# Performance work log

Measured on AMD Instinct MI355X. Metric: run time of the kernel, lower is better.

Reference implementation:

```python
import jax, jax.numpy as jnp
import numpy as np

N_NODES = 50000
N_EDGES = 800000
IN_CH = 128
OUT_CH = 64
HEADS = 4
NEG_SLOPE = 0.2


def setup_inputs() -> dict:
    key = jax.random.key(0)
    k1, k2, k3, k4, k5, k6 = jax.random.split(key, 6)
    x = jax.random.normal(k1, (N_NODES, IN_CH), dtype=jnp.float32)
    edge_index = jax.random.randint(k2, (2, N_EDGES), 0, N_NODES, dtype=jnp.int64)
    # GATConv params (glorot-ish scale)
    W = jax.random.normal(k3, (HEADS * OUT_CH, IN_CH), dtype=jnp.float32) * (1.0 / np.sqrt(IN_CH))
    att_src = jax.random.normal(k4, (HEADS, OUT_CH), dtype=jnp.float32) * 0.1
    att_dst = jax.random.normal(k5, (HEADS, OUT_CH), dtype=jnp.float32) * 0.1
    bias = jax.random.normal(k6, (HEADS * OUT_CH,), dtype=jnp.float32) * 0.01
    return {"x": x, "edge_index": edge_index, "W": W, "att_src": att_src, "att_dst": att_dst, "bias": bias}


def reference(x, edge_index, W, att_src, att_dst, bias):
    N = x.shape[0]
    H, C = att_src.shape
    # add self loops (PyG GATConv default add_self_loops=True)
    loops = jnp.arange(N, dtype=edge_index.dtype)
    src = jnp.concatenate([edge_index[0], loops])  # [E+N]
    dst = jnp.concatenate([edge_index[1], loops])
    # linear projection -> [N, H, C]
    xl = (x @ W.T).reshape(N, H, C)
    # per-node attention logits [N, H]
    a_src = jnp.einsum('nhc,hc->nh', xl, att_src)
    a_dst = jnp.einsum('nhc,hc->nh', xl, att_dst)
    # edge-wise score, leaky relu
    alpha = jax.nn.leaky_relu(a_src[src] + a_dst[dst], NEG_SLOPE)  # [E+N, H]
    # segment softmax over destination nodes (every node has a self loop -> no empty segments)
    amax = jax.ops.segment_max(alpha, dst, num_segments=N)
    e = jnp.exp(alpha - amax[dst])
    denom = jax.ops.segment_sum(e, dst, num_segments=N)
    coef = e / denom[dst]  # [E+N, H]
    # weighted scatter-aggregate of source features
    out = jax.ops.segment_sum(coef[:, :, None] * xl[src], dst, num_segments=N)  # [N, H, C]
    out = out.reshape(N, H * C) + bias
    # last_layer=False -> ELU activation
    return jax.nn.elu(out)
```

## Files before the change

### kernel.cpp

```cpp
#include <hip/hip_runtime.h>
#include <hip/hip_bf16.h>
#include <math.h>

#define IN_C 128
#define HC   256
#define CH   64
#define NEG  0.2f

typedef __attribute__((ext_vector_type(8))) short short8;
typedef __attribute__((ext_vector_type(4))) float f32x4;
typedef __attribute__((ext_vector_type(2))) float f32x2;

#define TSTRIDE 264

__device__ __forceinline__ float lrelu(float v) { return v > 0.f ? v : NEG * v; }

__device__ __forceinline__ unsigned short f2bf(float f) {
    __hip_bfloat16 h = __float2bfloat16(f);
    return *reinterpret_cast<unsigned short*>(&h);
}
__device__ __forceinline__ unsigned pack2(float lo, float hi) {
    return (unsigned)f2bf(lo) | ((unsigned)f2bf(hi) << 16);
}

__device__ __forceinline__ void fma8pk(f32x2* acc, float wf, const uint4 u) {
    const f32x2 w2 = {wf, wf};
    f32x2 b;
    b.x = __uint_as_float(u.x << 16); b.y = __uint_as_float(u.x & 0xFFFF0000u);
    acc[0] = __builtin_elementwise_fma(w2, b, acc[0]);
    b.x = __uint_as_float(u.y << 16); b.y = __uint_as_float(u.y & 0xFFFF0000u);
    acc[1] = __builtin_elementwise_fma(w2, b, acc[1]);
    b.x = __uint_as_float(u.z << 16); b.y = __uint_as_float(u.z & 0xFFFF0000u);
    acc[2] = __builtin_elementwise_fma(w2, b, acc[2]);
    b.x = __uint_as_float(u.w << 16); b.y = __uint_as_float(u.w & 0xFFFF0000u);
    acc[3] = __builtin_elementwise_fma(w2, b, acc[3]);
}

__global__ void k_wconv(const float* __restrict__ W, short* __restrict__ Wb, int n)
{
    int i = blockIdx.x * 256 + threadIdx.x;
    if (i * 4 >= n) return;
    const float4 v = *(const float4*)&W[i * 4];
    uint2 pk;
    pk.x = pack2(v.x, v.y);
    pk.y = pack2(v.z, v.w);
    *(uint2*)&Wb[i * 4] = pk;
}

__global__ void __launch_bounds__(256) k_gemm_deg(
    const float* __restrict__ x, const short* __restrict__ Wb,
    const float* __restrict__ att_src, const float* __restrict__ att_dst,
    const int* __restrict__ ei, int* __restrict__ deg, int* __restrict__ perm,
    __hip_bfloat16* __restrict__ xlb, float* __restrict__ asrc,
    float* __restrict__ adst, int N, int E, int DB)
{
    __shared__ short Wlds[256 * 128];

    const int t = threadIdx.x;

    if ((int)blockIdx.x < DB) {
        const int stride = DB * 256;
        for (int e = blockIdx.x * 256 + t; e < E; e += stride) {
            const int d = ei[E + e];
            perm[e] = atomicAdd(&deg[d], 1);
        }
        return;
    }

    const int bx   = blockIdx.x - DB;
    const int wv   = t >> 6;
    const int lane = t & 63;
    const int m    = lane & 15;
    const int quad = lane >> 4;
    const int r0   = bx * 64 + wv * 16;

#pragma unroll
    for (int i = 0; i < 16; ++i) {
        const int g   = t + 256 * i;
        const int row = g >> 4;
        const int c   = g & 15;
        const uint4 v = *(const uint4*)&Wb[g * 8];
        *(uint4*)&Wlds[row * 128 + ((c ^ (row & 15)) * 8)] = v;
    }
    __syncthreads();

    f32x4 acc[16];
#pragma unroll
    for (int tc = 0; tc < 16; ++tc) acc[tc] = (f32x4){0.f, 0.f, 0.f, 0.f};

    const int arow = min(r0 + m, N - 1);
    const float* xrow = &x[(size_t)arow * IN_C];

#pragma unroll
    for (int kc = 0; kc < IN_C; kc += 32) {
        union { short8 v; unsigned u[4]; } a;
        const float4 xa = *(const float4*)&xrow[kc + quad * 8];
        const float4 xb = *(const float4*)&xrow[kc + quad * 8 + 4];
        a.u[0] = pack2(xa.x, xa.y); a.u[1] = pack2(xa.z, xa.w);
        a.u[2] = pack2(xb.x, xb.y); a.u[3] = pack2(xb.z, xb.w);
        const int kchunk = (kc >> 3) + quad;
        const int slotoff = ((kchunk ^ m) * 8);
#pragma unroll
        for (int tc = 0; tc < 16; ++tc) {
            const short8 b = *(const short8*)&Wlds[(tc * 16 + m) * 128 + slotoff];
            acc[tc] = __builtin_amdgcn_mfma_f32_16x16x32_bf16(a.v, b, acc[tc], 0, 0, 0);
        }
    }

    float as_l[16], ad_l[16];
#pragma unroll
    for (int tc = 0; tc < 16; ++tc) {
        as_l[tc] = att_src[tc * 16 + m];
        ad_l[tc] = att_dst[tc * 16 + m];
    }
#pragma unroll
    for (int i = 0; i < 4; ++i) {
        const int grow = r0 + quad * 4 + i;
        const bool ok = grow < N;
        float ps[4] = {0.f, 0.f, 0.f, 0.f};
        float pd[4] = {0.f, 0.f, 0.f, 0.f};
#pragma unroll
        for (int tc = 0; tc < 16; ++tc) {
            const float v = acc[tc][i];
            ps[tc >> 2] = fmaf(v, as_l[tc], ps[tc >> 2]);
            pd[tc >> 2] = fmaf(v, ad_l[tc], pd[tc >> 2]);
        }
#pragma unroll
        for (int msk = 1; msk < 16; msk <<= 1) {
#pragma unroll
            for (int hd = 0; hd < 4; ++hd) {
                ps[hd] += __shfl_xor(ps[hd], msk);
                pd[hd] += __shfl_xor(pd[hd], msk);
            }
        }
        if (m == 0 && ok) {
#pragma unroll
            for (int hd = 0; hd < 4; ++hd) {
                asrc[grow * 4 + hd] = ps[hd];
                adst[grow * 4 + hd] = pd[hd];
            }
        }
    }

    __syncthreads();
#pragma unroll
    for (int i = 0; i < 4; ++i) {
        const int lrow = wv * 16 + quad * 4 + i;
#pragma unroll
        for (int tc = 0; tc < 16; ++tc)
            Wlds[lrow * TSTRIDE + tc * 16 + m] = (short)f2bf(acc[tc][i]);
    }
    __syncthreads();
    const int r0blk = bx * 64;
#pragma unroll
    for (int k2 = 0; k2 < 8; ++k2) {
        const int c   = t + 256 * k2;
        const int row = c >> 5;
        const int off = c & 31;
        if (r0blk + row < N) {
            const uint4 v = *(const uint4*)&Wlds[row * TSTRIDE + off * 8];
            *(uint4*)&xlb[(size_t)(r0blk + row) * HC + off * 8] = v;
        }
    }
}

__global__ void k_scan1(const int* __restrict__ deg, int* __restrict__ offs,
                        int* __restrict__ partials, int N)
{
    __shared__ int sh[1024];
    int t = threadIdx.x, b = blockIdx.x;
    int idx = b * 1024 + t;
    int v = (idx < N) ? deg[idx] : 0;
    sh[t] = v; __syncthreads();
    for (int off = 1; off < 1024; off <<= 1) {
        int u = (t >= off) ? sh[t - off] : 0;
        __syncthreads();
        sh[t] += u;
        __syncthreads();
    }
    if (idx < N) offs[idx] = sh[t] - v;
    if (t == 1023) partials[b] = sh[t];
}

__global__ void k_scan2(int* __restrict__ partials, int nparts)
{
    __shared__ int sh[1024];
    int t = threadIdx.x;
    int v = (t < nparts) ? partials[t] : 0;
    sh[t] = v; __syncthreads();
    for (int off = 1; off < 1024; off <<= 1) {
        int u = (t >= off) ? sh[t - off] : 0;
        __syncthreads();
        sh[t] += u;
        __syncthreads();
    }
    if (t < nparts) partials[t] = sh[t] - v;
}

__global__ void k_scan3(int* __restrict__ offs, const int* __restrict__ partials,
                        int N, int E)
{
    int t = threadIdx.x, b = blockIdx.x;
    int idx = b * 1024 + t;
    if (idx < N) offs[idx] += partials[b];
    if (idx == 0) offs[N] = E;
}

__global__ void k_place(const int* __restrict__ ei, const int* __restrict__ perm,
                        const int* __restrict__ offs, int* __restrict__ csr_src, int E)
{
    int e = blockIdx.x * 256 + threadIdx.x;
    if (e >= E) return;
    int s = ei[e];
    int d = ei[E + e];
    csr_src[offs[d] + perm[e]] = s;
}

__global__ void __launch_bounds__(256, 8) k_agg(
    const __hip_bfloat16* __restrict__ xlb, const float* __restrict__ asrc,
    const float* __restrict__ adst, const int* __restrict__ offs,
    const int* __restrict__ csr_src, const float* __restrict__ bias,
    float* __restrict__ out, int N)
{
    const int t    = threadIdx.x;
    const int wv   = t >> 6;
    const int lane = t & 63;
    const int half = lane >> 5;
    const int li   = lane & 31;
    const int h    = li >> 3;
    const int n    = blockIdx.x * 4 + wv;
    if (n >= N) return;

    const float adn = adst[n * 4 + h];
    const int   p0 = offs[n];
    const int   pe = offs[n + 1];

    f32x2 acc[4];
#pragma unroll
    for (int q = 0; q < 4; ++q) acc[q] = (f32x2){0.f, 0.f};
    float l = 0.f;

    if (half == 0) {
        const float w = __expf(lrelu(asrc[n * 4 + h] + adn));
        const uint4 u = *(const uint4*)&xlb[(unsigned)n * HC + li * 8];
        fma8pk(acc, w, u);
        l = w;
    }

    int p = p0 + half;

    for (; p + 16 <= pe + half; p += 16) {
        int s[8];
#pragma unroll
        for (int j = 0; j < 8; ++j) s[j] = csr_src[p + 2 * j];
        uint4 u[8];
#pragma unroll
        for (int j = 0; j < 8; ++j)
            u[j] = *(const uint4*)&xlb[(unsigned)s[j] * HC + li * 8];
        float w[4];
#pragma unroll
        for (int j = 0; j < 4; ++j)
            w[j] = __expf(lrelu(asrc[s[j] * 4 + h] + adn));
#pragma unroll
        for (int j = 0; j < 4; ++j) { l += w[j]; fma8pk(acc, w[j], u[j]); }
#pragma unroll
        for (int j = 0; j < 4; ++j)
            w[j] = __expf(lrelu(asrc[s[j + 4] * 4 + h] + adn));
#pragma unroll
        for (int j = 0; j < 4; ++j) { l += w[j]; fma8pk(acc, w[j], u[j + 4]); }
    }
    for (; p + 8 <= pe + half; p += 8) {
        int s[4];
#pragma unroll
        for (int j = 0; j < 4; ++j) s[j] = csr_src[p + 2 * j];
        uint4 u[4];
#pragma unroll
        for (int j = 0; j < 4; ++j)
            u[j] = *(const uint4*)&xlb[(unsigned)s[j] * HC + li * 8];
#pragma unroll
        for (int j = 0; j < 4; ++j) {
            const float w = __expf(lrelu(asrc[s[j] * 4 + h] + adn));
            l += w;
            fma8pk(acc, w, u[j]);
        }
    }
    for (; p < pe; p += 2) {
        const int s0 = csr_src[p];
        const uint4 u0 = *(const uint4*)&xlb[(unsigned)s0 * HC + li * 8];
        const float w0 = __expf(lrelu(asrc[s0 * 4 + h] + adn));
        l += w0;
        fma8pk(acc, w0, u0);
    }

    l += __shfl_xor(l, 32);
#pragma unroll
    for (int q = 0; q < 4; ++q) {
        acc[q].x += __shfl_xor(acc[q].x, 32);
        acc[q].y += __shfl_xor(acc[q].y, 32);
    }
    const float inv = 1.0f / l;

    const int cbase = li * 8 + half * 4;
    const float4 bv = *(const float4*)&bias[cbase];
    f32x4 o;
    o.x = acc[half * 2 + 0].x * inv + bv.x;
    o.y = acc[half * 2 + 0].y * inv + bv.y;
    o.z = acc[half * 2 + 1].x * inv + bv.z;
    o.w = acc[half * 2 + 1].y * inv + bv.w;
    o.x = o.x > 0.f ? o.x : expm1f(o.x);
    o.y = o.y > 0.f ? o.y : expm1f(o.y);
    o.z = o.z > 0.f ? o.z : expm1f(o.z);
    o.w = o.w > 0.f ? o.w : expm1f(o.w);
    __builtin_nontemporal_store(o, (f32x4*)&out[(size_t)n * HC + cbase]);
}

extern "C" void kernel_launch(void* const* d_in, const int* in_sizes, int n_in,
                              void* d_out, int out_size, void* d_ws, size_t ws_size,
                              hipStream_t stream) {
    const float* x       = (const float*)d_in[0];
    const int*   ei      = (const int*)d_in[1];
    const float* W       = (const float*)d_in[2];
    const float* att_src = (const float*)d_in[3];
    const float* att_dst = (const float*)d_in[4];
    const float* bias    = (const float*)d_in[5];
    float* out = (float*)d_out;

    const int N = in_sizes[0] / IN_C;
    const int E = in_sizes[1] / 2;
    const int W_ELEMS = HC * IN_C;

    char* p = (char*)d_ws;
    auto alloc = [&](size_t bytes) -> char* {
        char* q = p;
        p += (bytes + 255) & ~(size_t)255;
        return q;
    };
    __hip_bfloat16* xlb = (__hip_bfloat16*)alloc((size_t)N * HC * 2);
    short* Wb   = (short*)alloc((size_t)W_ELEMS * 2);
    float* asrc = (float*)alloc((size_t)N * 4 * 4);
    float* adst = (float*)alloc((size_t)N * 4 * 4);
    int*   deg  = (int*)alloc((size_t)N * 4);
    int*   offs = (int*)alloc((size_t)(N + 1) * 4);
    int*   perm = (int*)alloc((size_t)E * 4);
    int*   part = (int*)alloc(4096);
    int*   csr  = (int*)alloc((size_t)E * 4);

    (void)hipMemsetAsync(deg, 0, (size_t)N * 4, stream);

    k_wconv<<<(W_ELEMS / 4 + 255) / 256, 256, 0, stream>>>(W, Wb, W_ELEMS);

    const int GB = (N + 63) / 64;
    const int DB = (E + 2047) / 2048;
    k_gemm_deg<<<DB + GB, 256, 0, stream>>>(x, Wb, att_src, att_dst,
                                            ei, deg, perm, xlb, asrc, adst, N, E, DB);

    const int nb = (N + 1023) / 1024;
    k_scan1<<<nb, 1024, 0, stream>>>(deg, offs, part, N);
    k_scan2<<<1, 1024, 0, stream>>>(part, nb);
    k_scan3<<<nb, 1024, 0, stream>>>(offs, part, N, E);

    k_place<<<(E + 255) / 256, 256, 0, stream>>>(ei, perm, offs, csr, E);

    k_agg<<<(N + 3) / 4, 256, 0, stream>>>(xlb, asrc, adst, offs, csr, bias, out, N);
}
```

Baseline: 229.8 us.

## Fuse scan, CSR placement and aggregation into one cooperative persistent kernel

Replaces the three scan kernels, the placement kernel and the aggregation kernel with a single cooperative kernel. The phases are separated by grid-wide syncs, and aggregation becomes a persistent loop with 16 waves per 1024-thread block. This is meant to remove several kernel launch gaps and tail effects. In exchange it adds grid.sync barriers, and the large 1024-thread blocks may limit occupancy for the gather-heavy aggregation phase.

Result: slower. 382.5 us (+66.4%).

```diff
diff --git a/kernel.cpp b/kernel.cpp
--- a/kernel.cpp
+++ b/kernel.cpp
@@ -1,4 +1,5 @@
 #include <hip/hip_runtime.h>
+#include <hip/hip_cooperative_groups.h>
 #include <hip/hip_bf16.h>
 #include <math.h>
 
@@ -12,6 +13,8 @@
 typedef __attribute__((ext_vector_type(2))) float f32x2;
 
 #define TSTRIDE 264
+
+namespace cg = cooperative_groups;
 
 __device__ __forceinline__ float lrelu(float v) { return v > 0.f ? v : NEG * v; }
 
@@ -164,154 +167,153 @@
     }
 }
 
-__global__ void k_scan1(const int* __restrict__ deg, int* __restrict__ offs,
-                        int* __restrict__ partials, int N)
+__global__ void __launch_bounds__(1024, 8) k_post(
+    const __hip_bfloat16* __restrict__ xlb, const float* __restrict__ asrc,
+    const float* __restrict__ adst, const int* __restrict__ deg,
+    int* __restrict__ offs, int* __restrict__ part,
+    const int* __restrict__ perm, const int* __restrict__ ei,
+    int* __restrict__ csr, const float* __restrict__ bias,
+    float* __restrict__ out, int N, int E)
 {
     __shared__ int sh[1024];
-    int t = threadIdx.x, b = blockIdx.x;
-    int idx = b * 1024 + t;
-    int v = (idx < N) ? deg[idx] : 0;
-    sh[t] = v; __syncthreads();
-    for (int off = 1; off < 1024; off <<= 1) {
-        int u = (t >= off) ? sh[t - off] : 0;
+    const int t = threadIdx.x;
+    const int ntiles = (N + 1023) >> 10;
+    cg::grid_group grid = cg::this_grid();
+
+    for (int tile = blockIdx.x; tile < ntiles; tile += gridDim.x) {
+        const int idx = (tile << 10) + t;
+        const int v = (idx < N) ? deg[idx] : 0;
+        sh[t] = v; __syncthreads();
+        for (int off = 1; off < 1024; off <<= 1) {
+            const int u = (t >= off) ? sh[t - off] : 0;
+            __syncthreads();
+            sh[t] += u;
+            __syncthreads();
+        }
+        if (idx < N) offs[idx] = sh[t] - v;
+        if (t == 1023) part[tile] = sh[t];
         __syncthreads();
-        sh[t] += u;
-        __syncthreads();
-    }
-    if (idx < N) offs[idx] = sh[t] - v;
-    if (t == 1023) partials[b] = sh[t];
-}
-
-__global__ void k_scan2(int* __restrict__ partials, int nparts)
-{
-    __shared__ int sh[1024];
-    int t = threadIdx.x;
-    int v = (t < nparts) ? partials[t] : 0;
-    sh[t] = v; __syncthreads();
-    for (int off = 1; off < 1024; off <<= 1) {
-        int u = (t >= off) ? sh[t - off] : 0;
-        __syncthreads();
-        sh[t] += u;
-        __syncthreads();
-    }
-    if (t < nparts) partials[t] = sh[t] - v;
-}
-
-__global__ void k_scan3(int* __restrict__ offs, const int* __restrict__ partials,
-                        int N, int E)
-{
-    int t = threadIdx.x, b = blockIdx.x;
-    int idx = b * 1024 + t;
-    if (idx < N) offs[idx] += partials[b];
-    if (idx == 0) offs[N] = E;
-}
-
-__global__ void k_place(const int* __restrict__ ei, const int* __restrict__ perm,
-                        const int* __restrict__ offs, int* __restrict__ csr_src, int E)
-{
-    int e = blockIdx.x * 256 + threadIdx.x;
-    if (e >= E) return;
-    int s = ei[e];
-    int d = ei[E + e];
-    csr_src[offs[d] + perm[e]] = s;
-}
-
-__global__ void __launch_bounds__(256, 8) k_agg(
-    const __hip_bfloat16* __restrict__ xlb, const float* __restrict__ asrc,
-    const float* __restrict__ adst, const int* __restrict__ offs,
-    const int* __restrict__ csr_src, const float* __restrict__ bias,
-    float* __restrict__ out, int N)
-{
-    const int t    = threadIdx.x;
+    }
+    grid.sync();
+
+    if (blockIdx.x == 0) {
+        const int v = (t < ntiles) ? part[t] : 0;
+        sh[t] = v; __syncthreads();
+        for (int off = 1; off < 1024; off <<= 1) {
+            const int u = (t >= off) ? sh[t - off] : 0;
+            __syncthreads();
+            sh[t] += u;
+            __syncthreads();
+        }
+        if (t < ntiles) part[t] = sh[t] - v;
+    }
+    grid.sync();
+
+    for (int tile = blockIdx.x; tile < ntiles; tile += gridDim.x) {
+        const int idx = (tile << 10) + t;
+        if (idx < N) offs[idx] += part[tile];
+    }
+    if (blockIdx.x == 0 && t == 0) offs[N] = E;
+    grid.sync();
+
+    for (int e = blockIdx.x * 1024 + t; e < E; e += gridDim.x * 1024) {
+        const int s = ei[e];
+        const int d = ei[E + e];
+        csr[offs[d] + perm[e]] = s;
+    }
+    grid.sync();
+
     const int wv   = t >> 6;
     const int lane = t & 63;
     const int half = lane >> 5;
     const int li   = lane & 31;
     const int h    = li >> 3;
-    const int n    = blockIdx.x * 4 + wv;
-    if (n >= N) return;
-
-    const float adn = adst[n * 4 + h];
-    const int   p0 = offs[n];
-    const int   pe = offs[n + 1];
-
-    f32x2 acc[4];
-#pragma unroll
-    for (int q = 0; q < 4; ++q) acc[q] = (f32x2){0.f, 0.f};
-    float l = 0.f;
-
-    if (half == 0) {
-        const float w = __expf(lrelu(asrc[n * 4 + h] + adn));
-        const uint4 u = *(const uint4*)&xlb[(unsigned)n * HC + li * 8];
-        fma8pk(acc, w, u);
-        l = w;
-    }
-
-    int p = p0 + half;
-
-    for (; p + 16 <= pe + half; p += 16) {
-        int s[8];
-#pragma unroll
-        for (int j = 0; j < 8; ++j) s[j] = csr_src[p + 2 * j];
-        uint4 u[8];
-#pragma unroll
-        for (int j = 0; j < 8; ++j)
-            u[j] = *(const uint4*)&xlb[(unsigned)s[j] * HC + li * 8];
-        float w[4];
-#pragma unroll
-        for (int j = 0; j < 4; ++j)
-            w[j] = __expf(lrelu(asrc[s[j] * 4 + h] + adn));
-#pragma unroll
-        for (int j = 0; j < 4; ++j) { l += w[j]; fma8pk(acc, w[j], u[j]); }
-#pragma unroll
-        for (int j = 0; j < 4; ++j)
-            w[j] = __expf(lrelu(asrc[s[j + 4] * 4 + h] + adn));
-#pragma unroll
-        for (int j = 0; j < 4; ++j) { l += w[j]; fma8pk(acc, w[j], u[j + 4]); }
-    }
-    for (; p + 8 <= pe + half; p += 8) {
-        int s[4];
-#pragma unroll
-        for (int j = 0; j < 4; ++j) s[j] = csr_src[p + 2 * j];
-        uint4 u[4];
-#pragma unroll
-        for (int j = 0; j < 4; ++j)
-            u[j] = *(const uint4*)&xlb[(unsigned)s[j] * HC + li * 8];
-#pragma unroll
-        for (int j = 0; j < 4; ++j) {
-            const float w = __expf(lrelu(asrc[s[j] * 4 + h] + adn));
-            l += w;
-            fma8pk(acc, w, u[j]);
-        }
-    }
-    for (; p < pe; p += 2) {
-        const int s0 = csr_src[p];
-        const uint4 u0 = *(const uint4*)&xlb[(unsigned)s0 * HC + li * 8];
-        const float w0 = __expf(lrelu(asrc[s0 * 4 + h] + adn));
-        l += w0;
-        fma8pk(acc, w0, u0);
-    }
-
-    l += __shfl_xor(l, 32);
-#pragma unroll
-    for (int q = 0; q < 4; ++q) {
-        acc[q].x += __shfl_xor(acc[q].x, 32);
-        acc[q].y += __shfl_xor(acc[q].y, 32);
-    }
-    const float inv = 1.0f / l;
-
-    const int cbase = li * 8 + half * 4;
-    const float4 bv = *(const float4*)&bias[cbase];
-    f32x4 o;
-    o.x = acc[half * 2 + 0].x * inv + bv.x;
-    o.y = acc[half * 2 + 0].y * inv + bv.y;
-    o.z = acc[half * 2 + 1].x * inv + bv.z;
-    o.w = acc[half * 2 + 1].y * inv + bv.w;
-    o.x = o.x > 0.f ? o.x : expm1f(o.x);
-    o.y = o.y > 0.f ? o.y : expm1f(o.y);
-    o.z = o.z > 0.f ? o.z : expm1f(o.z);
-    o.w = o.w > 0.f ? o.w : expm1f(o.w);
-    __builtin_nontemporal_store(o, (f32x4*)&out[(size_t)n * HC + cbase]);
+    const int wave_id = blockIdx.x * 16 + wv;
+    const int nwaves  = gridDim.x * 16;
+
+    for (int n = wave_id; n < N; n += nwaves) {
+        const float adn = adst[n * 4 + h];
+        const int   p0 = offs[n];
+        const int   pe = offs[n + 1];
+
+        f32x2 acc[4];
+#pragma unroll
+        for (int q = 0; q < 4; ++q) acc[q] = (f32x2){0.f, 0.f};
+        float l = 0.f;
+
+        if (half == 0) {
+            const float w = __expf(lrelu(asrc[n * 4 + h] + adn));
+            const uint4 u = *(const uint4*)&xlb[(unsigned)n * HC + li * 8];
+            fma8pk(acc, w, u);
+            l = w;
+        }
+
+        int p = p0 + half;
+
+        for (; p + 16 <= pe + half; p += 16) {
+            int s[8];
+#pragma unroll
+            for (int j = 0; j < 8; ++j) s[j] = csr[p + 2 * j];
+            uint4 u[8];
+#pragma unroll
+            for (int j = 0; j < 8; ++j)
+                u[j] = *(const uint4*)&xlb[(unsigned)s[j] * HC + li * 8];
+            float w[4];
+#pragma unroll
+            for (int j = 0; j < 4; ++j)
+                w[j] = __expf(lrelu(asrc[s[j] * 4 + h] + adn));
+#pragma unroll
+            for (int j = 0; j < 4; ++j) { l += w[j]; fma8pk(acc, w[j], u[j]); }
+#pragma unroll
+            for (int j = 0; j < 4; ++j)
+                w[j] = __expf(lrelu(asrc[s[j + 4] * 4 + h] + adn));
+#pragma unroll
+            for (int j = 0; j < 4; ++j) { l += w[j]; fma8pk(acc, w[j], u[j + 4]); }
+        }
+        for (; p + 8 <= pe + half; p += 8) {
+            int s[4];
+#pragma unroll
+            for (int j = 0; j < 4; ++j) s[j] = csr[p + 2 * j];
+            uint4 u[4];
+#pragma unroll
+            for (int j = 0; j < 4; ++j)
+                u[j] = *(const uint4*)&xlb[(unsigned)s[j] * HC + li * 8];
+#pragma unroll
+            for (int j = 0; j < 4; ++j) {
+                const float w = __expf(lrelu(asrc[s[j] * 4 + h] + adn));
+                l += w;
+                fma8pk(acc, w, u[j]);
+            }
+        }
+        for (; p < pe; p += 2) {
+            const int s0 = csr[p];
+            const uint4 u0 = *(const uint4*)&xlb[(unsigned)s0 * HC + li * 8];
+            const float w0 = __expf(lrelu(asrc[s0 * 4 + h] + adn));
+            l += w0;
+            fma8pk(acc, w0, u0);
+        }
+
+        l += __shfl_xor(l, 32);
+#pragma unroll
+        for (int q = 0; q < 4; ++q) {
+            acc[q].x += __shfl_xor(acc[q].x, 32);
+            acc[q].y += __shfl_xor(acc[q].y, 32);
+        }
+        const float inv = 1.0f / l;
+
+        const int cbase = li * 8 + half * 4;
+        const float4 bv = *(const float4*)&bias[cbase];
+        f32x4 o;
+        o.x = acc[half * 2 + 0].x * inv + bv.x;
+        o.y = acc[half * 2 + 0].y * inv + bv.y;
+        o.z = acc[half * 2 + 1].x * inv + bv.z;
+        o.w = acc[half * 2 + 1].y * inv + bv.w;
+        o.x = o.x > 0.f ? o.x : expm1f(o.x);
+        o.y = o.y > 0.f ? o.y : expm1f(o.y);
+        o.z = o.z > 0.f ? o.z : expm1f(o.z);
+        o.w = o.w > 0.f ? o.w : expm1f(o.w);
+        __builtin_nontemporal_store(o, (f32x4*)&out[(size_t)n * HC + cbase]);
+    }
 }
 
 extern "C" void kernel_launch(void* const* d_in, const int* in_sizes, int n_in,
@@ -354,12 +356,21 @@
     k_gemm_deg<<<DB + GB, 256, 0, stream>>>(x, Wb, att_src, att_dst,
                                             ei, deg, perm, xlb, asrc, adst, N, E, DB);
 
-    const int nb = (N + 1023) / 1024;
-    k_scan1<<<nb, 1024, 0, stream>>>(deg, offs, part, N);
-    k_scan2<<<1, 1024, 0, stream>>>(part, nb);
-    k_scan3<<<nb, 1024, 0, stream>>>(offs, part, N, E);
-
-    k_place<<<(E + 255) / 256, 256, 0, stream>>>(ei, perm, offs, csr, E);
-
-    k_agg<<<(N + 3) / 4, 256, 0, stream>>>(xlb, asrc, adst, offs, csr, bias, out, N);
-}
+    static int coopBlocks = 0;
+    if (coopBlocks == 0) {
+        int perCU = 0;
+        (void)hipOccupancyMaxActiveBlocksPerMultiprocessor(&perCU, (const void*)k_post, 1024, 0);
+        if (perCU < 1) perCU = 1;
+        int numCU = 0;
+        (void)hipDeviceGetAttribute(&numCU, hipDeviceAttributeMultiprocessorCount, 0);
+        if (numCU <= 0) numCU = 256;
+        coopBlocks = perCU * numCU;
+    }
+
+    void* args[] = { (void*)&xlb, (void*)&asrc, (void*)&adst, (void*)&deg,
+                     (void*)&offs, (void*)&part, (void*)&perm, (void*)&ei,
+                     (void*)&csr, (void*)&bias, (void*)&out,
+                     (void*)&N, (void*)&E };
+    (void)hipLaunchCooperativeKernel((const void*)k_post, dim3(coopBlocks),
+                                     dim3(1024), args, 0, stream);
+}
```

## Fold weight conversion into GEMM and replace three-pass scan with decoupled lookback

Applied to the files above, without the earlier changes.

The separate fp32-to-bf16 weight conversion kernel is removed, and each GEMM block now converts W while staging it into shared memory. The three-kernel prefix scan over node degrees becomes a single-pass scan with decoupled lookback, using tile status words that are zeroed by the existing memset. This cuts three kernel launches and their serial dependencies, in exchange for redundant W conversion in every GEMM block and spin-waiting between scan tiles.

New measurement: 226.0 us. About the same (-1.7%).

```diff
diff --git a/kernel.cpp b/kernel.cpp
--- a/kernel.cpp
+++ b/kernel.cpp
@@ -36,19 +36,8 @@
     acc[3] = __builtin_elementwise_fma(w2, b, acc[3]);
 }
 
-__global__ void k_wconv(const float* __restrict__ W, short* __restrict__ Wb, int n)
-{
-    int i = blockIdx.x * 256 + threadIdx.x;
-    if (i * 4 >= n) return;
-    const float4 v = *(const float4*)&W[i * 4];
-    uint2 pk;
-    pk.x = pack2(v.x, v.y);
-    pk.y = pack2(v.z, v.w);
-    *(uint2*)&Wb[i * 4] = pk;
-}
-
 __global__ void __launch_bounds__(256) k_gemm_deg(
-    const float* __restrict__ x, const short* __restrict__ Wb,
+    const float* __restrict__ x, const float* __restrict__ W,
     const float* __restrict__ att_src, const float* __restrict__ att_dst,
     const int* __restrict__ ei, int* __restrict__ deg, int* __restrict__ perm,
     __hip_bfloat16* __restrict__ xlb, float* __restrict__ asrc,
@@ -79,7 +68,11 @@
         const int g   = t + 256 * i;
         const int row = g >> 4;
         const int c   = g & 15;
-        const uint4 v = *(const uint4*)&Wb[g * 8];
+        const float4 wa = *(const float4*)&W[g * 8];
+        const float4 wb = *(const float4*)&W[g * 8 + 4];
+        uint4 v;
+        v.x = pack2(wa.x, wa.y); v.y = pack2(wa.z, wa.w);
+        v.z = pack2(wb.x, wb.y); v.w = pack2(wb.z, wb.w);
         *(uint4*)&Wlds[row * 128 + ((c ^ (row & 15)) * 8)] = v;
     }
     __syncthreads();
@@ -164,46 +157,69 @@
     }
 }
 
-__global__ void k_scan1(const int* __restrict__ deg, int* __restrict__ offs,
-                        int* __restrict__ partials, int N)
+#define SCAN_TILE 2048
+__global__ void __launch_bounds__(256) k_scan(
+    const int* __restrict__ deg, int* __restrict__ offs,
+    unsigned long long* __restrict__ tstat, int N, int E, int ntiles)
 {
-    __shared__ int sh[1024];
-    int t = threadIdx.x, b = blockIdx.x;
-    int idx = b * 1024 + t;
-    int v = (idx < N) ? deg[idx] : 0;
-    sh[t] = v; __syncthreads();
-    for (int off = 1; off < 1024; off <<= 1) {
-        int u = (t >= off) ? sh[t - off] : 0;
+    __shared__ int sh[256];
+    __shared__ int sh_base;
+    const int tile = blockIdx.x;
+    const int t = threadIdx.x;
+    const int base = tile * SCAN_TILE + t * 8;
+
+    int v[8];
+    int tsum = 0;
+#pragma unroll
+    for (int j = 0; j < 8; ++j) {
+        const int idx = base + j;
+        v[j] = (idx < N) ? deg[idx] : 0;
+        tsum += v[j];
+    }
+    sh[t] = tsum;
+    __syncthreads();
+    for (int off = 1; off < 256; off <<= 1) {
+        const int u = (t >= off) ? sh[t - off] : 0;
         __syncthreads();
         sh[t] += u;
         __syncthreads();
     }
-    if (idx < N) offs[idx] = sh[t] - v;
-    if (t == 1023) partials[b] = sh[t];
-}
-
-__global__ void k_scan2(int* __restrict__ partials, int nparts)
-{
-    __shared__ int sh[1024];
-    int t = threadIdx.x;
-    int v = (t < nparts) ? partials[t] : 0;
-    sh[t] = v; __syncthreads();
-    for (int off = 1; off < 1024; off <<= 1) {
-        int u = (t >= off) ? sh[t - off] : 0;
-        __syncthreads();
-        sh[t] += u;
-        __syncthreads();
-    }
-    if (t < nparts) partials[t] = sh[t] - v;
-}
-
-__global__ void k_scan3(int* __restrict__ offs, const int* __restrict__ partials,
-                        int N, int E)
-{
-    int t = threadIdx.x, b = blockIdx.x;
-    int idx = b * 1024 + t;
-    if (idx < N) offs[idx] += partials[b];
-    if (idx == 0) offs[N] = E;
+    const int blockSum = sh[255];
+    const int texcl = sh[t] - tsum;
+
+    if (t == 0) {
+        int excl = 0;
+        if (tile == 0) {
+            __hip_atomic_store(&tstat[0], (2ull << 32) | (unsigned)blockSum,
+                               __ATOMIC_RELEASE, __HIP_MEMORY_SCOPE_AGENT);
+        } else {
+            __hip_atomic_store(&tstat[tile], (1ull << 32) | (unsigned)blockSum,
+                               __ATOMIC_RELEASE, __HIP_MEMORY_SCOPE_AGENT);
+            int pb = tile - 1;
+            while (true) {
+                const unsigned long long st = __hip_atomic_load(&tstat[pb],
+                        __ATOMIC_ACQUIRE, __HIP_MEMORY_SCOPE_AGENT);
+                const unsigned state = (unsigned)(st >> 32);
+                if (state == 0u) continue;
+                excl += (int)(unsigned)(st & 0xFFFFFFFFu);
+                if (state == 2u) break;
+                --pb;
+            }
+            __hip_atomic_store(&tstat[tile],
+                               (2ull << 32) | (unsigned)(excl + blockSum),
+                               __ATOMIC_RELEASE, __HIP_MEMORY_SCOPE_AGENT);
+        }
+        sh_base = excl;
+    }
+    __syncthreads();
+    int running = sh_base + texcl;
+#pragma unroll
+    for (int j = 0; j < 8; ++j) {
+        const int idx = base + j;
+        if (idx < N) offs[idx] = running;
+        running += v[j];
+    }
+    if (tile == ntiles - 1 && t == 255) offs[N] = E;
 }
 
 __global__ void k_place(const int* __restrict__ ei, const int* __restrict__ perm,
@@ -327,7 +343,6 @@
 
     const int N = in_sizes[0] / IN_C;
     const int E = in_sizes[1] / 2;
-    const int W_ELEMS = HC * IN_C;
 
     char* p = (char*)d_ws;
     auto alloc = [&](size_t bytes) -> char* {
@@ -336,28 +351,24 @@
         return q;
     };
     __hip_bfloat16* xlb = (__hip_bfloat16*)alloc((size_t)N * HC * 2);
-    short* Wb   = (short*)alloc((size_t)W_ELEMS * 2);
     float* asrc = (float*)alloc((size_t)N * 4 * 4);
     float* adst = (float*)alloc((size_t)N * 4 * 4);
     int*   deg  = (int*)alloc((size_t)N * 4);
+    unsigned long long* tstat = (unsigned long long*)alloc(4096);
     int*   offs = (int*)alloc((size_t)(N + 1) * 4);
     int*   perm = (int*)alloc((size_t)E * 4);
-    int*   part = (int*)alloc(4096);
     int*   csr  = (int*)alloc((size_t)E * 4);
 
-    (void)hipMemsetAsync(deg, 0, (size_t)N * 4, stream);
-
-    k_wconv<<<(W_ELEMS / 4 + 255) / 256, 256, 0, stream>>>(W, Wb, W_ELEMS);
+    const size_t degpad = ((size_t)N * 4 + 255) & ~(size_t)255;
+    (void)hipMemsetAsync(deg, 0, degpad + 4096, stream);
 
     const int GB = (N + 63) / 64;
     const int DB = (E + 2047) / 2048;
-    k_gemm_deg<<<DB + GB, 256, 0, stream>>>(x, Wb, att_src, att_dst,
+    k_gemm_deg<<<DB + GB, 256, 0, stream>>>(x, W, att_src, att_dst,
                                             ei, deg, perm, xlb, asrc, adst, N, E, DB);
 
-    const int nb = (N + 1023) / 1024;
-    k_scan1<<<nb, 1024, 0, stream>>>(deg, offs, part, N);
-    k_scan2<<<1, 1024, 0, stream>>>(part, nb);
-    k_scan3<<<nb, 1024, 0, stream>>>(offs, part, N, E);
+    const int ntiles = (N + SCAN_TILE - 1) / SCAN_TILE;
+    k_scan<<<ntiles, 256, 0, stream>>>(deg, offs, tstat, N, E, ntiles);
 
     k_place<<<(E + 255) / 256, 256, 0, stream>>>(ei, perm, offs, csr, E);
 
```
